# Kernel tuning notes

Measured on AMD Instinct MI355X. Metric: run time of the kernel, lower is better.

## Reference

```python
import jax, jax.numpy as jnp
import numpy as np

N_NODES = 50000
N_EDGES = 600000
N_GRAPHS = 64
IN_C, HID_C, OUT_C = 128, 128, 64


def gcn_conv(x, edge_index, W, b, num_nodes):
    """PyG GCNConv: x' = D^-1/2 (A + I) D^-1/2 (x W) + b, messages src->dst."""
    src, dst = edge_index[0], edge_index[1]
    # add self-loops
    loop = jnp.arange(num_nodes, dtype=src.dtype)
    src_full = jnp.concatenate([src, loop])
    dst_full = jnp.concatenate([dst, loop])
    # degree of A+I counted at the aggregation (dst) side
    deg = jax.ops.segment_sum(jnp.ones_like(dst_full, dtype=x.dtype), dst_full,
                              num_segments=num_nodes)
    dinv = jax.lax.rsqrt(jnp.maximum(deg, 1.0))
    norm = dinv[src_full] * dinv[dst_full]              # [E+N]
    h = x @ W                                           # [N, C_out] dense GEMM
    msg = h[src_full] * norm[:, None]                   # gather + scale
    out = jax.ops.segment_sum(msg, dst_full, num_segments=num_nodes)  # scatter-add
    return out + b


def global_mean_pool(x, batch, num_graphs):
    s = jax.ops.segment_sum(x, batch, num_segments=num_graphs)
    cnt = jax.ops.segment_sum(jnp.ones_like(batch, dtype=x.dtype), batch,
                              num_segments=num_graphs)
    return s / jnp.maximum(cnt, 1.0)[:, None]


def setup_inputs() -> dict:
    key = jax.random.key(0)
    ks = jax.random.split(key, 8)
    x = jax.random.normal(ks[0], (N_NODES, IN_C), dtype=jnp.float32)
    edge_index = jax.random.randint(ks[1], (2, N_EDGES), 0, N_NODES, dtype=jnp.int64)
    batch = jnp.sort(jax.random.randint(ks[2], (N_NODES,), 0, N_GRAPHS, dtype=jnp.int64))
    # Glorot-style init like PyG defaults
    W1 = jax.random.normal(ks[3], (IN_C, HID_C), dtype=jnp.float32) * (1.0 / np.sqrt(IN_C))
    b1 = jnp.zeros((HID_C,), dtype=jnp.float32)
    W2 = jax.random.normal(ks[4], (HID_C, OUT_C), dtype=jnp.float32) * (1.0 / np.sqrt(HID_C))
    b2 = jnp.zeros((OUT_C,), dtype=jnp.float32)
    return {"x": x, "W1": W1, "b1": b1, "W2": W2, "b2": b2,
            "edge_index": edge_index, "batch": batch}


def reference(x, W1, b1, W2, b2, edge_index, batch):
    h = gcn_conv(x, edge_index, W1, b1, N_NODES)
    h = jax.nn.relu(h)
    h = gcn_conv(h, edge_index, W2, b2, N_NODES)
    return global_mean_pool(h, batch, N_GRAPHS)  # [N_GRAPHS, OUT_C]
```

## Files before the change

kernel.cpp:

```cpp
#include <hip/hip_runtime.h>

#define NN 50000
#define NE 600000
#define NG 64
#define SCAN_T 1024
#define SCAN_NB ((NN + SCAN_T - 1) / SCAN_T)
#define PSPLIT 16

typedef unsigned int uint_t;
typedef unsigned short ushort_t;

__device__ __forceinline__ ushort_t f2bf(float x) {
    uint_t u = __builtin_bit_cast(uint_t, x);
    u = (u + 0x7FFFu + ((u >> 16) & 1u)) >> 16;
    return (ushort_t)u;
}
__device__ __forceinline__ float bf_lo(uint_t p) {
    uint_t v = p << 16; return __builtin_bit_cast(float, v);
}
__device__ __forceinline__ float bf_hi(uint_t p) {
    uint_t v = p & 0xFFFF0000u; return __builtin_bit_cast(float, v);
}

__global__ void k_zero_deg(int* __restrict__ deg) {
    int i = blockIdx.x * blockDim.x + threadIdx.x;
    if (i < NN) deg[i] = 0;
}

__global__ void k_hist(const int* __restrict__ dst, int* __restrict__ deg) {
    int e = blockIdx.x * blockDim.x + threadIdx.x;
    if (e < NE) atomicAdd(&deg[dst[e]], 1);
}

__global__ __launch_bounds__(SCAN_T) void k_scan1(const int* __restrict__ deg,
                                                  int* __restrict__ blockSums) {
    __shared__ int s[SCAN_T];
    int i = blockIdx.x * SCAN_T + threadIdx.x;
    s[threadIdx.x] = (i < NN) ? deg[i] : 0;
    __syncthreads();
    for (int off = SCAN_T / 2; off > 0; off >>= 1) {
        if (threadIdx.x < off) s[threadIdx.x] += s[threadIdx.x + off];
        __syncthreads();
    }
    if (threadIdx.x == 0) blockSums[blockIdx.x] = s[0];
}

__global__ void k_scan2(const int* __restrict__ blockSums, int* __restrict__ blockOffs) {
    int t = threadIdx.x;
    int orig = (t < SCAN_NB) ? blockSums[t] : 0;
    int v = orig;
    for (int off = 1; off < 64; off <<= 1) {
        int u = __shfl_up(v, off);
        if (t >= off) v += u;
    }
    if (t < SCAN_NB) blockOffs[t] = v - orig;
}

__global__ __launch_bounds__(SCAN_T) void k_scan3(const int* __restrict__ deg,
                                                  const int* __restrict__ blockOffs,
                                                  int* __restrict__ rowptr,
                                                  int* __restrict__ cursor,
                                                  float* __restrict__ dinv) {
    __shared__ int s[SCAN_T];
    const int t = threadIdx.x;
    const int i = blockIdx.x * SCAN_T + t;
    const int v = (i < NN) ? deg[i] : 0;
    s[t] = v;
    __syncthreads();
    for (int off = 1; off < SCAN_T; off <<= 1) {
        int u = (t >= off) ? s[t - off] : 0;
        int cur = s[t];
        __syncthreads();
        s[t] = cur + u;
        __syncthreads();
    }
    if (i < NN) {
        int ex = blockOffs[blockIdx.x] + s[t] - v;
        rowptr[i] = ex;
        cursor[i] = ex;
        dinv[i] = rsqrtf((float)(v + 1));
    }
    if (i == 0) rowptr[NN] = NE;
}

__global__ void k_scatter(const int* __restrict__ src, const int* __restrict__ dst,
                          int* __restrict__ cursor, int* __restrict__ csr_src) {
    int e = blockIdx.x * blockDim.x + threadIdx.x;
    if (e >= NE) return;
    int d = dst[e];
    int p = atomicAdd(&cursor[d], 1);
    csr_src[p] = src[e];
}

template <int CIN, int COUT, int RPT>
__global__ __launch_bounds__(256) void k_gemm(const float* __restrict__ X,
                                              const float* __restrict__ W,
                                              const float* __restrict__ dinv,
                                              ushort_t* __restrict__ Hb) {
    constexpr int TPR = COUT / 4;
    constexpr int NGRP = 256 / TPR;
    constexpr int BM = NGRP * RPT;
    constexpr int LDW = CIN + 4;
    constexpr int F4R = CIN / 4;
    __shared__ float xs[BM][LDW];
    const int tid = threadIdx.x;
    const int row0 = blockIdx.x * BM;

    for (int idx = tid; idx < BM * F4R; idx += 256) {
        int r = idx / F4R, c4 = idx % F4R;
        int row = row0 + r;
        float4 v = make_float4(0.f, 0.f, 0.f, 0.f);
        if (row < NN) v = ((const float4*)X)[(long)row * F4R + c4];
        *(float4*)&xs[r][c4 * 4] = v;
    }
    __syncthreads();

    const int g = tid / TPR;
    const int j = (tid % TPR) * 4;
    const int r0 = g * RPT;

    float4 acc[RPT];
#pragma unroll
    for (int r = 0; r < RPT; ++r) acc[r] = make_float4(0.f, 0.f, 0.f, 0.f);

    for (int k = 0; k < CIN; k += 4) {
        const float4 w0 = *(const float4*)&W[(k + 0) * COUT + j];
        const float4 w1 = *(const float4*)&W[(k + 1) * COUT + j];
        const float4 w2 = *(const float4*)&W[(k + 2) * COUT + j];
        const float4 w3 = *(const float4*)&W[(k + 3) * COUT + j];
#pragma unroll
        for (int r = 0; r < RPT; ++r) {
            const float4 xv = *(const float4*)&xs[r0 + r][k];
            acc[r].x += xv.x * w0.x + xv.y * w1.x + xv.z * w2.x + xv.w * w3.x;
            acc[r].y += xv.x * w0.y + xv.y * w1.y + xv.z * w2.y + xv.w * w3.y;
            acc[r].z += xv.x * w0.z + xv.y * w1.z + xv.z * w2.z + xv.w * w3.z;
            acc[r].w += xv.x * w0.w + xv.y * w1.w + xv.z * w2.w + xv.w * w3.w;
        }
    }

#pragma unroll
    for (int r = 0; r < RPT; ++r) {
        int row = row0 + r0 + r;
        if (row < NN) {
            float sc = dinv[row];
            ushort4 o;
            o.x = f2bf(acc[r].x * sc);
            o.y = f2bf(acc[r].y * sc);
            o.z = f2bf(acc[r].z * sc);
            o.w = f2bf(acc[r].w * sc);
            *(ushort4*)&Hb[(long)row * COUT + j] = o;
        }
    }
}

template <int C, int EPI>
__global__ __launch_bounds__(256) void k_agg(const int* __restrict__ rowptr,
                                             const int* __restrict__ csr_src,
                                             const float* __restrict__ dinv,
                                             const ushort_t* __restrict__ Hb,
                                             const float* __restrict__ bias,
                                             void* __restrict__ OUT) {
    constexpr int TPN = C / 8;
    constexpr int NPB = 256 / TPN;
    const int node = blockIdx.x * NPB + threadIdx.x / TPN;
    if (node >= NN) return;
    const int lane = threadIdx.x % TPN;
    const float dd = dinv[node];
    const uint4* __restrict__ H4 = (const uint4*)Hb;

    float a0, a1, a2, a3, a4, a5, a6, a7;
    {
        uint4 sv = H4[(long)node * TPN + lane];
        a0 = bf_lo(sv.x); a1 = bf_hi(sv.x);
        a2 = bf_lo(sv.y); a3 = bf_hi(sv.y);
        a4 = bf_lo(sv.z); a5 = bf_hi(sv.z);
        a6 = bf_lo(sv.w); a7 = bf_hi(sv.w);
    }

    const int beg = rowptr[node], end = rowptr[node + 1];
    int k = beg;
    const int n4 = beg + ((end - beg) & ~3);
    for (; k < n4; k += 4) {
        int s0 = csr_src[k + 0];
        int s1 = csr_src[k + 1];
        int s2 = csr_src[k + 2];
        int s3 = csr_src[k + 3];
        uint4 h0 = H4[(long)s0 * TPN + lane];
        uint4 h1 = H4[(long)s1 * TPN + lane];
        uint4 h2 = H4[(long)s2 * TPN + lane];
        uint4 h3 = H4[(long)s3 * TPN + lane];
        a0 += (bf_lo(h0.x) + bf_lo(h1.x)) + (bf_lo(h2.x) + bf_lo(h3.x));
        a1 += (bf_hi(h0.x) + bf_hi(h1.x)) + (bf_hi(h2.x) + bf_hi(h3.x));
        a2 += (bf_lo(h0.y) + bf_lo(h1.y)) + (bf_lo(h2.y) + bf_lo(h3.y));
        a3 += (bf_hi(h0.y) + bf_hi(h1.y)) + (bf_hi(h2.y) + bf_hi(h3.y));
        a4 += (bf_lo(h0.z) + bf_lo(h1.z)) + (bf_lo(h2.z) + bf_lo(h3.z));
        a5 += (bf_hi(h0.z) + bf_hi(h1.z)) + (bf_hi(h2.z) + bf_hi(h3.z));
        a6 += (bf_lo(h0.w) + bf_lo(h1.w)) + (bf_lo(h2.w) + bf_lo(h3.w));
        a7 += (bf_hi(h0.w) + bf_hi(h1.w)) + (bf_hi(h2.w) + bf_hi(h3.w));
    }
    for (; k < end; ++k) {
        int s = csr_src[k];
        uint4 h = H4[(long)s * TPN + lane];
        a0 += bf_lo(h.x); a1 += bf_hi(h.x);
        a2 += bf_lo(h.y); a3 += bf_hi(h.y);
        a4 += bf_lo(h.z); a5 += bf_hi(h.z);
        a6 += bf_lo(h.w); a7 += bf_hi(h.w);
    }

    a0 *= dd; a1 *= dd; a2 *= dd; a3 *= dd;
    a4 *= dd; a5 *= dd; a6 *= dd; a7 *= dd;

    if (EPI == 0) {
        const float4 b0 = *(const float4*)&bias[lane * 8];
        const float4 b1 = *(const float4*)&bias[lane * 8 + 4];
        a0 = fmaxf(a0 + b0.x, 0.f) * dd; a1 = fmaxf(a1 + b0.y, 0.f) * dd;
        a2 = fmaxf(a2 + b0.z, 0.f) * dd; a3 = fmaxf(a3 + b0.w, 0.f) * dd;
        a4 = fmaxf(a4 + b1.x, 0.f) * dd; a5 = fmaxf(a5 + b1.y, 0.f) * dd;
        a6 = fmaxf(a6 + b1.z, 0.f) * dd; a7 = fmaxf(a7 + b1.w, 0.f) * dd;
        uint4 o;
        o.x = (uint_t)f2bf(a0) | ((uint_t)f2bf(a1) << 16);
        o.y = (uint_t)f2bf(a2) | ((uint_t)f2bf(a3) << 16);
        o.z = (uint_t)f2bf(a4) | ((uint_t)f2bf(a5) << 16);
        o.w = (uint_t)f2bf(a6) | ((uint_t)f2bf(a7) << 16);
        ((uint4*)OUT)[(long)node * TPN + lane] = o;
    } else {
        float* o = (float*)OUT + (long)node * C + lane * 8;
        *(float4*)(o + 0) = make_float4(a0, a1, a2, a3);
        *(float4*)(o + 4) = make_float4(a4, a5, a6, a7);
    }
}

template <int C>
__global__ __launch_bounds__(256) void k_pool1(const float* __restrict__ H,
                                               const int* __restrict__ batch,
                                               float* __restrict__ partial) {
    constexpr int F4 = C / 4;
    constexpr int SUB = 256 / F4;
    const int g = blockIdx.x / PSPLIT;
    const int s = blockIdx.x % PSPLIT;
    int beg, end;
    {
        int lo = 0, hi = NN;
        while (lo < hi) { int mid = (lo + hi) >> 1; if (batch[mid] < g) lo = mid + 1; else hi = mid; }
        beg = lo;
        lo = beg; hi = NN;
        while (lo < hi) { int mid = (lo + hi) >> 1; if (batch[mid] < g + 1) lo = mid + 1; else hi = mid; }
        end = lo;
    }
    const int c4 = threadIdx.x % F4;
    const int rg = threadIdx.x / F4;
    const float4* __restrict__ H4 = (const float4*)H;

    float4 acc = make_float4(0.f, 0.f, 0.f, 0.f);
    for (int n = beg + s * SUB + rg; n < end; n += PSPLIT * SUB) {
        float4 h = H4[(long)n * F4 + c4];
        acc.x += h.x; acc.y += h.y; acc.z += h.z; acc.w += h.w;
    }
    __shared__ float4 red[SUB][F4 + 1];
    red[rg][c4] = acc;
    __syncthreads();
    if (rg == 0) {
        float4 t = red[0][c4];
#pragma unroll
        for (int i = 1; i < SUB; ++i) {
            float4 u = red[i][c4];
            t.x += u.x; t.y += u.y; t.z += u.z; t.w += u.w;
        }
        ((float4*)partial)[(long)blockIdx.x * F4 + c4] = t;
    }
}

__global__ __launch_bounds__(128) void k_pool2gemm(const float* __restrict__ partial,
                                                   const int* __restrict__ batch,
                                                   const float* __restrict__ W2,
                                                   const float* __restrict__ b2,
                                                   float* __restrict__ out) {
    const int g = blockIdx.x;
    const int t = threadIdx.x;
    int beg, end;
    {
        int lo = 0, hi = NN;
        while (lo < hi) { int mid = (lo + hi) >> 1; if (batch[mid] < g) lo = mid + 1; else hi = mid; }
        beg = lo;
        lo = beg; hi = NN;
        while (lo < hi) { int mid = (lo + hi) >> 1; if (batch[mid] < g + 1) lo = mid + 1; else hi = mid; }
        end = lo;
    }
    const int cnt = end - beg;
    __shared__ float P[128];
    float s = 0.f;
    for (int i = 0; i < PSPLIT; ++i) s += partial[(long)(g * PSPLIT + i) * 128 + t];
    P[t] = (cnt > 0) ? s / (float)cnt : 0.f;
    __syncthreads();
    if (t < 64) {
        float acc = 0.f;
        for (int k = 0; k < 128; ++k) acc += P[k] * W2[k * 64 + t];
        out[g * 64 + t] = (cnt > 0) ? acc + b2[t] : 0.f;
    }
}

extern "C" void kernel_launch(void* const* d_in, const int* in_sizes, int n_in,
                              void* d_out, int out_size, void* d_ws, size_t ws_size,
                              hipStream_t stream) {
    const float* x  = (const float*)d_in[0];
    const float* W1 = (const float*)d_in[1];
    const float* b1 = (const float*)d_in[2];
    const float* W2 = (const float*)d_in[3];
    const float* b2 = (const float*)d_in[4];
    const int* ei   = (const int*)d_in[5];
    const int* src  = ei;
    const int* dst  = ei + NE;
    const int* batch = (const int*)d_in[6];
    float* out = (float*)d_out;

    char* p = (char*)d_ws;
    int* deg       = (int*)p;          p += (size_t)NN * 4;
    int* rowptr    = (int*)p;          p += (size_t)(NN + 4) * 4;
    int* cursor    = (int*)p;          p += (size_t)NN * 4;
    int* csr_src   = (int*)p;          p += (size_t)NE * 4;
    int* blockSums = (int*)p;          p += (size_t)64 * 4;
    int* blockOffs = (int*)p;          p += (size_t)64 * 4;
    float* dinv    = (float*)p;        p += (size_t)NN * 4;
    float* partial = (float*)p;        p += (size_t)NG * PSPLIT * 128 * 4;
    ushort_t* Hb   = (ushort_t*)p;     p += (size_t)NN * 128 * 2;
    ushort_t* H1b  = (ushort_t*)p;     p += (size_t)NN * 128 * 2;
    float* bufV    = (float*)p;        p += (size_t)NN * 128 * 4;

    k_zero_deg<<<(NN + 255) / 256, 256, 0, stream>>>(deg);
    k_hist<<<(NE + 255) / 256, 256, 0, stream>>>(dst, deg);
    k_scan1<<<SCAN_NB, SCAN_T, 0, stream>>>(deg, blockSums);
    k_scan2<<<1, 64, 0, stream>>>(blockSums, blockOffs);
    k_scan3<<<SCAN_NB, SCAN_T, 0, stream>>>(deg, blockOffs, rowptr, cursor, dinv);
    k_scatter<<<(NE + 255) / 256, 256, 0, stream>>>(src, dst, cursor, csr_src);

    k_gemm<128, 128, 8><<<(NN + 63) / 64, 256, 0, stream>>>(x, W1, dinv, Hb);
    k_agg<128, 0><<<(NN + 15) / 16, 256, 0, stream>>>(rowptr, csr_src, dinv, Hb, b1, H1b);

    k_agg<128, 1><<<(NN + 15) / 16, 256, 0, stream>>>(rowptr, csr_src, dinv, H1b, b1 , bufV);

    k_pool1<128><<<NG * PSPLIT, 256, 0, stream>>>(bufV, batch, partial);
    k_pool2gemm<<<NG, 128, 0, stream>>>(partial, batch, W2, b2, out);
}
```

Before: 187.7 us.

## Use bf16 MFMA for first-layer GEMM and store second aggregation in bf16

Replaces the scalar FP32 GEMM with a bf16 MFMA 16x16x32 kernel. X and a pre-transposed bf16 W1 are staged in XOR-swizzled shared memory, with 128-row tiles per block. A small prep kernel converts W1 to transposed bf16. The second aggregation now writes bf16 instead of fp32, and the pooling kernel reads bf16, which halves that intermediate traffic. This lowers precision of X, W1 and the layer-2 aggregate, and the MFMA epilogue stores scalar 2-byte values with a strided pattern.

Result: faster. 168.0 us (-10.5%).

```diff
diff --git a/kernel.cpp b/kernel.cpp
--- a/kernel.cpp
+++ b/kernel.cpp
@@ -9,6 +9,8 @@
 
 typedef unsigned int uint_t;
 typedef unsigned short ushort_t;
+typedef __attribute__((ext_vector_type(8))) short bf16x8;
+typedef __attribute__((ext_vector_type(4))) float f32x4;
 
 __device__ __forceinline__ ushort_t f2bf(float x) {
     uint_t u = __builtin_bit_cast(uint_t, x);
@@ -92,63 +94,83 @@
     csr_src[p] = src[e];
 }
 
-template <int CIN, int COUT, int RPT>
-__global__ __launch_bounds__(256) void k_gemm(const float* __restrict__ X,
-                                              const float* __restrict__ W,
-                                              const float* __restrict__ dinv,
-                                              ushort_t* __restrict__ Hb) {
-    constexpr int TPR = COUT / 4;
-    constexpr int NGRP = 256 / TPR;
-    constexpr int BM = NGRP * RPT;
-    constexpr int LDW = CIN + 4;
-    constexpr int F4R = CIN / 4;
-    __shared__ float xs[BM][LDW];
+__global__ void k_wprep(const float* __restrict__ W, ushort_t* __restrict__ Wt) {
+    int idx = blockIdx.x * 256 + threadIdx.x;
+    if (idx >= 128 * 128) return;
+    int k = idx >> 7, n = idx & 127;
+    Wt[n * 128 + k] = f2bf(W[idx]);
+}
+
+__global__ __launch_bounds__(256) void k_gemm_mfma(const float* __restrict__ X,
+                                                   const ushort_t* __restrict__ Wt,
+                                                   const float* __restrict__ dinv,
+                                                   ushort_t* __restrict__ Hb) {
+    __shared__ ushort_t xs[128 * 128];
+    __shared__ ushort_t ws[128 * 128];
     const int tid = threadIdx.x;
-    const int row0 = blockIdx.x * BM;
-
-    for (int idx = tid; idx < BM * F4R; idx += 256) {
-        int r = idx / F4R, c4 = idx % F4R;
+    const int row0 = blockIdx.x * 128;
+
+    for (int idx = tid; idx < 128 * 32; idx += 256) {
+        int r = idx >> 5, c4 = idx & 31;
         int row = row0 + r;
         float4 v = make_float4(0.f, 0.f, 0.f, 0.f);
-        if (row < NN) v = ((const float4*)X)[(long)row * F4R + c4];
-        *(float4*)&xs[r][c4 * 4] = v;
-    }
-    __syncthreads();
-
-    const int g = tid / TPR;
-    const int j = (tid % TPR) * 4;
-    const int r0 = g * RPT;
-
-    float4 acc[RPT];
-#pragma unroll
-    for (int r = 0; r < RPT; ++r) acc[r] = make_float4(0.f, 0.f, 0.f, 0.f);
-
-    for (int k = 0; k < CIN; k += 4) {
-        const float4 w0 = *(const float4*)&W[(k + 0) * COUT + j];
-        const float4 w1 = *(const float4*)&W[(k + 1) * COUT + j];
-        const float4 w2 = *(const float4*)&W[(k + 2) * COUT + j];
-        const float4 w3 = *(const float4*)&W[(k + 3) * COUT + j];
-#pragma unroll
-        for (int r = 0; r < RPT; ++r) {
-            const float4 xv = *(const float4*)&xs[r0 + r][k];
-            acc[r].x += xv.x * w0.x + xv.y * w1.x + xv.z * w2.x + xv.w * w3.x;
-            acc[r].y += xv.x * w0.y + xv.y * w1.y + xv.z * w2.y + xv.w * w3.y;
-            acc[r].z += xv.x * w0.z + xv.y * w1.z + xv.z * w2.z + xv.w * w3.z;
-            acc[r].w += xv.x * w0.w + xv.y * w1.w + xv.z * w2.w + xv.w * w3.w;
+        if (row < NN) v = ((const float4*)X)[(long)row * 32 + c4];
+        ushort4 o;
+        o.x = f2bf(v.x); o.y = f2bf(v.y); o.z = f2bf(v.z); o.w = f2bf(v.w);
+        uint_t byte = (uint_t)(r * 256 + c4 * 8) ^ (uint_t)((r & 7) << 4);
+        *(ushort4*)((char*)xs + byte) = o;
+    }
+    for (int idx = tid; idx < 128 * 16; idx += 256) {
+        int n = idx >> 4, c16 = idx & 15;
+        uint4 v = ((const uint4*)Wt)[idx];
+        uint_t byte = (uint_t)(n * 256 + c16 * 16) ^ (uint_t)((n & 7) << 4);
+        *(uint4*)((char*)ws + byte) = v;
+    }
+    __syncthreads();
+
+    const int w = tid >> 6;
+    const int l = tid & 63;
+    const int m0 = (w >> 1) * 4;
+    const int n0 = (w & 1) * 4;
+    const int lr = l & 15;
+    const int kg = l >> 4;
+
+    f32x4 acc[4][4] = {};
+    for (int kk = 0; kk < 4; ++kk) {
+        const int kb = kk * 64 + kg * 16;
+        bf16x8 a[4], b[4];
+#pragma unroll
+        for (int m = 0; m < 4; ++m) {
+            int r = (m0 + m) * 16 + lr;
+            uint_t byte = (uint_t)(r * 256 + kb) ^ (uint_t)((r & 7) << 4);
+            a[m] = *(const bf16x8*)((const char*)xs + byte);
         }
-    }
-
-#pragma unroll
-    for (int r = 0; r < RPT; ++r) {
-        int row = row0 + r0 + r;
-        if (row < NN) {
-            float sc = dinv[row];
-            ushort4 o;
-            o.x = f2bf(acc[r].x * sc);
-            o.y = f2bf(acc[r].y * sc);
-            o.z = f2bf(acc[r].z * sc);
-            o.w = f2bf(acc[r].w * sc);
-            *(ushort4*)&Hb[(long)row * COUT + j] = o;
+#pragma unroll
+        for (int n = 0; n < 4; ++n) {
+            int r = (n0 + n) * 16 + lr;
+            uint_t byte = (uint_t)(r * 256 + kb) ^ (uint_t)((r & 7) << 4);
+            b[n] = *(const bf16x8*)((const char*)ws + byte);
+        }
+#pragma unroll
+        for (int m = 0; m < 4; ++m)
+#pragma unroll
+            for (int n = 0; n < 4; ++n)
+                acc[m][n] = __builtin_amdgcn_mfma_f32_16x16x32_bf16(a[m], b[n], acc[m][n], 0, 0, 0);
+    }
+
+#pragma unroll
+    for (int m = 0; m < 4; ++m) {
+#pragma unroll
+        for (int r = 0; r < 4; ++r) {
+            int row = row0 + (m0 + m) * 16 + kg * 4 + r;
+            if (row < NN) {
+                float sc = dinv[row];
+#pragma unroll
+                for (int n = 0; n < 4; ++n) {
+                    int col = (n0 + n) * 16 + lr;
+                    Hb[(long)row * 128 + col] = f2bf(acc[m][n][r] * sc);
+                }
+            }
         }
     }
 }
@@ -217,25 +239,18 @@
         a2 = fmaxf(a2 + b0.z, 0.f) * dd; a3 = fmaxf(a3 + b0.w, 0.f) * dd;
         a4 = fmaxf(a4 + b1.x, 0.f) * dd; a5 = fmaxf(a5 + b1.y, 0.f) * dd;
         a6 = fmaxf(a6 + b1.z, 0.f) * dd; a7 = fmaxf(a7 + b1.w, 0.f) * dd;
-        uint4 o;
-        o.x = (uint_t)f2bf(a0) | ((uint_t)f2bf(a1) << 16);
-        o.y = (uint_t)f2bf(a2) | ((uint_t)f2bf(a3) << 16);
-        o.z = (uint_t)f2bf(a4) | ((uint_t)f2bf(a5) << 16);
-        o.w = (uint_t)f2bf(a6) | ((uint_t)f2bf(a7) << 16);
-        ((uint4*)OUT)[(long)node * TPN + lane] = o;
-    } else {
-        float* o = (float*)OUT + (long)node * C + lane * 8;
-        *(float4*)(o + 0) = make_float4(a0, a1, a2, a3);
-        *(float4*)(o + 4) = make_float4(a4, a5, a6, a7);
-    }
-}
-
-template <int C>
-__global__ __launch_bounds__(256) void k_pool1(const float* __restrict__ H,
+    }
+    uint4 o;
+    o.x = (uint_t)f2bf(a0) | ((uint_t)f2bf(a1) << 16);
+    o.y = (uint_t)f2bf(a2) | ((uint_t)f2bf(a3) << 16);
+    o.z = (uint_t)f2bf(a4) | ((uint_t)f2bf(a5) << 16);
+    o.w = (uint_t)f2bf(a6) | ((uint_t)f2bf(a7) << 16);
+    ((uint4*)OUT)[(long)node * TPN + lane] = o;
+}
+
+__global__ __launch_bounds__(256) void k_pool1(const ushort_t* __restrict__ V,
                                                const int* __restrict__ batch,
                                                float* __restrict__ partial) {
-    constexpr int F4 = C / 4;
-    constexpr int SUB = 256 / F4;
     const int g = blockIdx.x / PSPLIT;
     const int s = blockIdx.x % PSPLIT;
     int beg, end;
@@ -247,26 +262,27 @@
         while (lo < hi) { int mid = (lo + hi) >> 1; if (batch[mid] < g + 1) lo = mid + 1; else hi = mid; }
         end = lo;
     }
-    const int c4 = threadIdx.x % F4;
-    const int rg = threadIdx.x / F4;
-    const float4* __restrict__ H4 = (const float4*)H;
+    const int c = threadIdx.x & 31;
+    const int rg = threadIdx.x >> 5;
+    const uint2* __restrict__ V2 = (const uint2*)V;
 
     float4 acc = make_float4(0.f, 0.f, 0.f, 0.f);
-    for (int n = beg + s * SUB + rg; n < end; n += PSPLIT * SUB) {
-        float4 h = H4[(long)n * F4 + c4];
-        acc.x += h.x; acc.y += h.y; acc.z += h.z; acc.w += h.w;
-    }
-    __shared__ float4 red[SUB][F4 + 1];
-    red[rg][c4] = acc;
+    for (int n = beg + s * 8 + rg; n < end; n += PSPLIT * 8) {
+        uint2 h = V2[(long)n * 32 + c];
+        acc.x += bf_lo(h.x); acc.y += bf_hi(h.x);
+        acc.z += bf_lo(h.y); acc.w += bf_hi(h.y);
+    }
+    __shared__ float4 red[8][33];
+    red[rg][c] = acc;
     __syncthreads();
     if (rg == 0) {
-        float4 t = red[0][c4];
-#pragma unroll
-        for (int i = 1; i < SUB; ++i) {
-            float4 u = red[i][c4];
+        float4 t = red[0][c];
+#pragma unroll
+        for (int i = 1; i < 8; ++i) {
+            float4 u = red[i][c];
             t.x += u.x; t.y += u.y; t.z += u.z; t.w += u.w;
         }
-        ((float4*)partial)[(long)blockIdx.x * F4 + c4] = t;
+        ((float4*)partial)[(long)blockIdx.x * 32 + c] = t;
     }
 }
 
@@ -322,10 +338,12 @@
     int* blockOffs = (int*)p;          p += (size_t)64 * 4;
     float* dinv    = (float*)p;        p += (size_t)NN * 4;
     float* partial = (float*)p;        p += (size_t)NG * PSPLIT * 128 * 4;
+    ushort_t* Wt   = (ushort_t*)p;     p += (size_t)128 * 128 * 2;
     ushort_t* Hb   = (ushort_t*)p;     p += (size_t)NN * 128 * 2;
     ushort_t* H1b  = (ushort_t*)p;     p += (size_t)NN * 128 * 2;
-    float* bufV    = (float*)p;        p += (size_t)NN * 128 * 4;
-
+    ushort_t* Vb   = (ushort_t*)p;     p += (size_t)NN * 128 * 2;
+
+    k_wprep<<<64, 256, 0, stream>>>(W1, Wt);
     k_zero_deg<<<(NN + 255) / 256, 256, 0, stream>>>(deg);
     k_hist<<<(NE + 255) / 256, 256, 0, stream>>>(dst, deg);
     k_scan1<<<SCAN_NB, SCAN_T, 0, stream>>>(deg, blockSums);
@@ -333,11 +351,11 @@
     k_scan3<<<SCAN_NB, SCAN_T, 0, stream>>>(deg, blockOffs, rowptr, cursor, dinv);
     k_scatter<<<(NE + 255) / 256, 256, 0, stream>>>(src, dst, cursor, csr_src);
 
-    k_gemm<128, 128, 8><<<(NN + 63) / 64, 256, 0, stream>>>(x, W1, dinv, Hb);
+    k_gemm_mfma<<<(NN + 127) / 128, 256, 0, stream>>>(x, Wt, dinv, Hb);
     k_agg<128, 0><<<(NN + 15) / 16, 256, 0, stream>>>(rowptr, csr_src, dinv, Hb, b1, H1b);
 
-    k_agg<128, 1><<<(NN + 15) / 16, 256, 0, stream>>>(rowptr, csr_src, dinv, H1b, b1 , bufV);
-
-    k_pool1<128><<<NG * PSPLIT, 256, 0, stream>>>(bufV, batch, partial);
+    k_agg<128, 1><<<(NN + 15) / 16, 256, 0, stream>>>(rowptr, csr_src, dinv, H1b, b1 , Vb);
+
+    k_pool1<<<NG * PSPLIT, 256, 0, stream>>>(Vb, batch, partial);
     k_pool2gemm<<<NG, 128, 0, stream>>>(partial, batch, W2, b2, out);
 }
```
